# Kernel tuning notes

Measured on AMD Instinct MI355X. Metric: run time of the kernel, lower is better.

Reference implementation:

```python
import jax, jax.numpy as jnp
import numpy as np

N_NODES = 100000
N_EDGES = 1600000
D_IN = 128
D_HID = 128
D_OUT = 128


def setup_inputs() -> dict:
    key = jax.random.key(0)
    ks = jax.random.split(key, 12)
    x = jax.random.normal(ks[0], (N_NODES, D_IN), dtype=jnp.float32)
    edge_index = jax.random.randint(ks[1], (2, N_EDGES), 0, N_NODES, dtype=jnp.int64)
    s = 0.05
    # GraphConv layer l: out = agg @ w_rel + x @ w_root + b  (lin_rel has bias, lin_root does not)
    w_rel1 = jax.random.normal(ks[2], (D_IN, D_HID), dtype=jnp.float32) * s
    w_root1 = jax.random.normal(ks[3], (D_IN, D_HID), dtype=jnp.float32) * s
    b1 = jax.random.normal(ks[4], (D_HID,), dtype=jnp.float32) * s
    w_rel2 = jax.random.normal(ks[5], (D_HID, D_HID), dtype=jnp.float32) * s
    w_root2 = jax.random.normal(ks[6], (D_HID, D_HID), dtype=jnp.float32) * s
    b2 = jax.random.normal(ks[7], (D_HID,), dtype=jnp.float32) * s
    w_rel3 = jax.random.normal(ks[8], (D_HID, D_OUT), dtype=jnp.float32) * s
    w_root3 = jax.random.normal(ks[9], (D_HID, D_OUT), dtype=jnp.float32) * s
    b3 = jax.random.normal(ks[10], (D_OUT,), dtype=jnp.float32) * s
    return {"x": x, "edge_index": edge_index,
            "w_rel1": w_rel1, "w_root1": w_root1, "b1": b1,
            "w_rel2": w_rel2, "w_root2": w_root2, "b2": b2,
            "w_rel3": w_rel3, "w_root3": w_root3, "b3": b3}


def _graph_conv(h, src, dst, w_rel, w_root, b):
    # sum-aggregate neighbor features (message = x_j, flow src -> dst),
    # then linear; identical math to PyG GraphConv with aggr='add'.
    agg = jax.ops.segment_sum(h[src], dst, num_segments=h.shape[0])
    return agg @ w_rel + h @ w_root + b


def reference(x, edge_index, w_rel1, w_root1, b1, w_rel2, w_root2, b2, w_rel3, w_root3, b3):
    src, dst = edge_index[0], edge_index[1]
    h = jax.nn.relu(_graph_conv(x, src, dst, w_rel1, w_root1, b1))
    h = jax.nn.relu(_graph_conv(h, src, dst, w_rel2, w_root2, b2))
    out = _graph_conv(h, src, dst, w_rel3, w_root3, b3)
    return out
```

## Files before the change

kernel.cpp:

```cpp
#include <hip/hip_runtime.h>
#include <hip/hip_bf16.h>
#include <stdint.h>

typedef __hip_bfloat16 bf16;
typedef __hip_bfloat162 bf162;

typedef __attribute__((ext_vector_type(8))) short short8;
typedef __attribute__((ext_vector_type(4))) float floatx4;

#define BSH   8
#define BSZ   256
#define CHUNK 8192
#define NBMAX 512


__device__ __forceinline__ void acc2(float& a, float& b, unsigned u) {
    a += __uint_as_float(u << 16);
    b += __uint_as_float(u & 0xffff0000u);
}

__global__ __launch_bounds__(256)
void prep_bhist_kernel(const float* __restrict__ x, bf16* __restrict__ y, int n4, int nCvt,
                       const float* __restrict__ wr1, const float* __restrict__ wo1,
                       const float* __restrict__ wr2, const float* __restrict__ wo2,
                       const float* __restrict__ wr3, const float* __restrict__ wo3,
                       bf16* __restrict__ w1, bf16* __restrict__ w2, bf16* __restrict__ w3,
                       const int* __restrict__ dst, int* __restrict__ T,
                       int E, int NB, int GB) {
    __shared__ int lh[NBMAX];
    const int b = blockIdx.x;
    if (b < nCvt) {
        const int i = b * 256 + threadIdx.x;
        if (i < n4) {
            float4 v = ((const float4*)x)[i];
            bf162 a, c;
            a.x = __float2bfloat16(v.x); a.y = __float2bfloat16(v.y);
            c.x = __float2bfloat16(v.z); c.y = __float2bfloat16(v.w);
            ((bf162*)y)[i * 2]     = a;
            ((bf162*)y)[i * 2 + 1] = c;
        }
        return;
    }
    if (b < nCvt + 48) {
        int t = (b - nCvt) * 256 + threadIdx.x;
        const int layer = t >> 12;
        t &= 4095;
        const float* wrel  = (layer == 0) ? wr1 : (layer == 1) ? wr2 : wr3;
        const float* wroot = (layer == 0) ? wo1 : (layer == 1) ? wo2 : wo3;
        bf16*        wsw   = (layer == 0) ? w1  : (layer == 1) ? w2  : w3;
        const int lane = t & 63;
        const int ct   = (t >> 6) & 7;
        const int kt   = t >> 9;
        const int kbase = kt * 32 + (lane >> 4) * 8;
        const int n     = ct * 16 + (lane & 15);
        bf16* q = wsw + (size_t)t * 8;
#pragma unroll
        for (int j = 0; j < 8; ++j) {
            const int k = kbase + j;
            const float v = (k < 128) ? wrel[k * 128 + n] : wroot[(k - 128) * 128 + n];
            q[j] = __float2bfloat16(v);
        }
        return;
    }
    const int bb = b - nCvt - 48;
    for (int u = threadIdx.x; u < NB; u += 256) lh[u] = 0;
    __syncthreads();
    const int beg = bb * CHUNK, end = min(beg + CHUNK, E);
    for (int e = beg + threadIdx.x; e < end; e += 256)
        atomicAdd(&lh[dst[e] >> BSH], 1);
    __syncthreads();
    for (int u = threadIdx.x; u < NB; u += 256)
        T[u * GB + bb] = lh[u];
}


__global__ __launch_bounds__(256)
void scan1_kernel(const int* __restrict__ deg, int* __restrict__ rp,
                  int* __restrict__ bsum, int n) {
    __shared__ int s[256];
    const int tid = threadIdx.x;
    const int i = blockIdx.x * 256 + tid;
    const int d = (i < n) ? deg[i] : 0;
    s[tid] = d;
    __syncthreads();
    for (int off = 1; off < 256; off <<= 1) {
        int u = (tid >= off) ? s[tid - off] : 0;
        __syncthreads();
        s[tid] += u;
        __syncthreads();
    }
    if (i < n) rp[i] = s[tid] - d;
    if (tid == 255) bsum[blockIdx.x] = s[255];
}

__global__ __launch_bounds__(512)
void scan2_kernel(int* __restrict__ bsum, int G) {
    __shared__ int s[512];
    const int tid = threadIdx.x;
    const int d = (tid < G) ? bsum[tid] : 0;
    s[tid] = d;
    __syncthreads();
    for (int off = 1; off < 512; off <<= 1) {
        int u = (tid >= off) ? s[tid - off] : 0;
        __syncthreads();
        s[tid] += u;
        __syncthreads();
    }
    if (tid < G) bsum[tid] = s[tid] - d;
}


__global__ __launch_bounds__(256)
void bscatter_kernel(const int* __restrict__ src, const int* __restrict__ dst,
                     const int* __restrict__ T, const int* __restrict__ bsum,
                     int* __restrict__ ebuf, int E, int NB, int GB) {
    __shared__ int lofs[NBMAX];
    const int b = blockIdx.x;
    for (int u = threadIdx.x; u < NB; u += 256) {
        const int idx = u * GB + b;
        lofs[u] = T[idx] + bsum[idx >> 8];
    }
    __syncthreads();
    const int beg = b * CHUNK, end = min(beg + CHUNK, E);
    for (int e = beg + threadIdx.x; e < end; e += 256) {
        const int d = dst[e];
        const int u = d >> BSH;
        const int pos = atomicAdd(&lofs[u], 1);
        ebuf[pos] = (src[e] << BSH) | (d & (BSZ - 1));
    }
}

__global__ __launch_bounds__(256)
void bbuild_kernel(const int* __restrict__ T, const int* __restrict__ bsum,
                   const int* __restrict__ ebuf,
                   int* __restrict__ rp, int* __restrict__ col,
                   int E, int N, int NB, int GB) {
    __shared__ int s[256];
    __shared__ int lrank[256];
    const int u = blockIdx.x;
    const int tid = threadIdx.x;
    const int i0 = u * GB;
    const int beg = T[i0] + bsum[i0 >> 8];
    const int i1 = (u + 1) * GB;
    const int end = (u + 1 < NB) ? (T[i1] + bsum[i1 >> 8]) : E;

    lrank[tid] = 0;
    __syncthreads();
    for (int e = beg + tid; e < end; e += 256)
        atomicAdd(&lrank[ebuf[e] & (BSZ - 1)], 1);
    __syncthreads();
    const int cntv = lrank[tid];
    s[tid] = cntv;
    __syncthreads();
    for (int off = 1; off < 256; off <<= 1) {
        int v = (tid >= off) ? s[tid - off] : 0;
        __syncthreads();
        s[tid] += v;
        __syncthreads();
    }
    const int excl = s[tid] - cntv;
    const int node = u * BSZ + tid;
    if (node < N) rp[node] = beg + excl;
    if (u == NB - 1 && tid == 0) rp[N] = E;
    lrank[tid] = beg + excl;
    __syncthreads();
    for (int e = beg + tid; e < end; e += 256) {
        const int p = ebuf[e];
        const int pos = atomicAdd(&lrank[p & (BSZ - 1)], 1);
        col[pos] = p >> BSH;
    }
}


__global__ __launch_bounds__(512)
void agg_kernel(const bf16* __restrict__ h, const int* __restrict__ rp,
                const int* __restrict__ col, bf16* __restrict__ agg, int N) {
    const int lane = threadIdx.x & 63;
    const int wid  = threadIdx.x >> 6;
    const int node = blockIdx.x * 8 + wid;
    if (node >= N) return;
    const int half = lane >> 5;
    const int l32  = lane & 31;
    const int f    = l32 * 4;
    const int beg = rp[node], end = rp[node + 1];

    float acc[4] = {0.f, 0.f, 0.f, 0.f};
    int e = beg;
#pragma unroll 2
    for (; e + 8 <= end; e += 8) {
        const int s0 = col[e + half];
        const int s1 = col[e + 2 + half];
        const int s2 = col[e + 4 + half];
        const int s3 = col[e + 6 + half];
        const uint2 r0 = *(const uint2*)(h + (size_t)s0 * 128 + f);
        const uint2 r1 = *(const uint2*)(h + (size_t)s1 * 128 + f);
        const uint2 r2 = *(const uint2*)(h + (size_t)s2 * 128 + f);
        const uint2 r3 = *(const uint2*)(h + (size_t)s3 * 128 + f);
        acc2(acc[0], acc[1], r0.x); acc2(acc[2], acc[3], r0.y);
        acc2(acc[0], acc[1], r1.x); acc2(acc[2], acc[3], r1.y);
        acc2(acc[0], acc[1], r2.x); acc2(acc[2], acc[3], r2.y);
        acc2(acc[0], acc[1], r3.x); acc2(acc[2], acc[3], r3.y);
    }
    for (; e < end; e += 2) {
        const bool act = (e + half) < end;
        const int s = col[act ? (e + half) : e];
        const uint2 r = *(const uint2*)(h + (size_t)s * 128 + f);
        if (act) { acc2(acc[0], acc[1], r.x); acc2(acc[2], acc[3], r.y); }
    }
#pragma unroll
    for (int j = 0; j < 4; ++j)
        acc[j] += __shfl_xor(acc[j], 32, 64);
    if (half == 0) {
        bf162 o0, o1;
        o0.x = __float2bfloat16(acc[0]); o0.y = __float2bfloat16(acc[1]);
        o1.x = __float2bfloat16(acc[2]); o1.y = __float2bfloat16(acc[3]);
        bf162* q = (bf162*)(agg + (size_t)node * 128 + f);
        q[0] = o0;
        q[1] = o1;
    }
}


template <bool RELU, typename OT>
__global__ __launch_bounds__(512)
void mfma_gemm_kernel(const bf16* __restrict__ Aagg, const bf16* __restrict__ Hroot,
                      const bf16* __restrict__ wsw, const float* __restrict__ bias,
                      OT* __restrict__ out, int M) {
    __shared__ __align__(16) char smem[67584];
    const int tid = threadIdx.x;

#pragma unroll
    for (int i = 0; i < 8; ++i) {
        const int off = i * 8192 + tid * 16;
        *(float4*)(smem + off) = *(const float4*)((const char*)wsw + off);
    }
    __syncthreads();

    const int lane = tid & 63;
    const int wave = tid >> 6;
    const int l15  = lane & 15;
    const int quad = lane >> 4;
    const int base = blockIdx.x * 128;
    const int row_a = base + wave * 16 + l15;
    const bool rowok = row_a < M;
    const bf16* wl = (const bf16*)smem;

    floatx4 acc[8];
#pragma unroll
    for (int ct = 0; ct < 8; ++ct) acc[ct] = (floatx4){0.f, 0.f, 0.f, 0.f};

#pragma unroll
    for (int kt = 0; kt < 8; ++kt) {
        const bf16* Abase = (kt < 4) ? Aagg : Hroot;
        const int k0 = (kt & 3) * 32 + quad * 8;
        short8 afrag = (short8){0, 0, 0, 0, 0, 0, 0, 0};
        if (rowok) afrag = *(const short8*)(Abase + (size_t)row_a * 128 + k0);
#pragma unroll
        for (int ct = 0; ct < 8; ++ct) {
            const short8 bfrag = *(const short8*)(wl + (size_t)((kt * 8 + ct) * 64 + lane) * 8);
            acc[ct] = __builtin_amdgcn_mfma_f32_16x16x32_bf16(afrag, bfrag, acc[ct], 0, 0, 0);
        }
    }

    __syncthreads();
    const int rloc = wave * 16 + quad * 4;

    if constexpr (sizeof(OT) == 2) {
        bf16* tl = (bf16*)smem;
#pragma unroll
        for (int ct = 0; ct < 8; ++ct) {
            const int colc = ct * 16 + l15;
            const float bv = bias[colc];
#pragma unroll
            for (int r = 0; r < 4; ++r) {
                float v = acc[ct][r] + bv;
                if (RELU) v = fmaxf(v, 0.f);
                tl[(rloc + r) * 136 + colc] = __float2bfloat16(v);
            }
        }
        __syncthreads();
#pragma unroll
        for (int i = 0; i < 4; ++i) {
            const int chunk = i * 512 + tid;
            const int row = chunk >> 4;
            const int c   = chunk & 15;
            if (base + row < M)
                *(float4*)((char*)out + (size_t)(base + row) * 256 + c * 16) =
                    *(const float4*)(smem + row * 272 + c * 16);
        }
    } else {
        float* tl = (float*)smem;
#pragma unroll
        for (int ct = 0; ct < 8; ++ct) {
            const int colc = ct * 16 + l15;
            const float bv = bias[colc];
#pragma unroll
            for (int r = 0; r < 4; ++r) {
                float v = acc[ct][r] + bv;
                if (RELU) v = fmaxf(v, 0.f);
                tl[(rloc + r) * 132 + colc] = v;
            }
        }
        __syncthreads();
#pragma unroll
        for (int i = 0; i < 8; ++i) {
            const int chunk = i * 512 + tid;
            const int row = chunk >> 5;
            const int c   = chunk & 31;
            if (base + row < M)
                *(float4*)((char*)out + (size_t)(base + row) * 512 + c * 16) =
                    *(const float4*)(smem + row * 528 + c * 16);
        }
    }
}


extern "C" void kernel_launch(void* const* d_in, const int* in_sizes, int n_in,
                              void* d_out, int out_size, void* d_ws, size_t ws_size,
                              hipStream_t stream) {
    const float* x       = (const float*)d_in[0];
    const int*   ei      = (const int*)d_in[1];
    const float* w_rel1  = (const float*)d_in[2];
    const float* w_root1 = (const float*)d_in[3];
    const float* b1      = (const float*)d_in[4];
    const float* w_rel2  = (const float*)d_in[5];
    const float* w_root2 = (const float*)d_in[6];
    const float* b2      = (const float*)d_in[7];
    const float* w_rel3  = (const float*)d_in[8];
    const float* w_root3 = (const float*)d_in[9];
    const float* b3      = (const float*)d_in[10];
    float* out = (float*)d_out;

    const int N = in_sizes[0] / 128;
    const int E = in_sizes[1] / 2;
    const int* src = ei;
    const int* dst = ei + E;

    char* w = (char*)d_ws;
    auto alloc = [&](size_t bytes) {
        char* p = w;
        w += (bytes + 255) & ~(size_t)255;
        return p;
    };
    int*  col  = (int*)alloc((size_t)E * 4);
    int*  rp   = (int*)alloc((size_t)(N + 1) * 4);
    bf16* h1   = (bf16*)alloc((size_t)N * 128 * 2);
    bf16* xbf  = (bf16*)alloc((size_t)N * 128 * 2);
    bf16* aggb = (bf16*)alloc((size_t)N * 128 * 2);
    bf16* wsw1 = (bf16*)alloc(32768 * 2);
    bf16* wsw2 = (bf16*)alloc(32768 * 2);
    bf16* wsw3 = (bf16*)alloc(32768 * 2);
    bf16* h2   = xbf;
    int*  T    = (int*)h1;
    int*  bsum = (int*)(h1 + 1024 * 1024);
    int*  ebuf = (int*)aggb;

    const int NB = (N + BSZ - 1) / BSZ;
    const int GB = (E + CHUNK - 1) / CHUNK;
    const int nT = NB * GB;
    const int scanTBlocks = (nT + 255) / 256;

    const int aggBlocks  = (N + 7) / 8;
    const int gemmBlocks = (N + 127) / 128;
    const int cvtBlocks  = (N * 32 + 255) / 256;

    prep_bhist_kernel<<<cvtBlocks + 48 + GB, 256, 0, stream>>>(
        x, xbf, N * 32, cvtBlocks,
        w_rel1, w_root1, w_rel2, w_root2, w_rel3, w_root3,
        wsw1, wsw2, wsw3,
        dst, T, E, NB, GB);

    scan1_kernel<<<scanTBlocks, 256, 0, stream>>>(T, T, bsum, nT);
    scan2_kernel<<<1, 512, 0, stream>>>(bsum, scanTBlocks);
    bscatter_kernel<<<GB, 256, 0, stream>>>(src, dst, T, bsum, ebuf, E, NB, GB);
    bbuild_kernel<<<NB, 256, 0, stream>>>(T, bsum, ebuf, rp, col, E, N, NB, GB);

    agg_kernel<<<aggBlocks, 512, 0, stream>>>(xbf, rp, col, aggb, N);
    mfma_gemm_kernel<true, bf16><<<gemmBlocks, 512, 0, stream>>>(aggb, xbf, wsw1, b1, h1, N);
    agg_kernel<<<aggBlocks, 512, 0, stream>>>(h1, rp, col, aggb, N);
    mfma_gemm_kernel<true, bf16><<<gemmBlocks, 512, 0, stream>>>(aggb, h1, wsw2, b2, h2, N);
    agg_kernel<<<aggBlocks, 512, 0, stream>>>(h2, rp, col, aggb, N);
    mfma_gemm_kernel<false, float><<<gemmBlocks, 512, 0, stream>>>(aggb, h2, wsw3, b3, out, N);
}
```

Baseline: 425.9 us.

## Store bf16 features in 16-column slabs so each aggregation block gathers from one slab

```diff
diff --git a/kernel.cpp b/kernel.cpp
--- a/kernel.cpp
+++ b/kernel.cpp
@@ -12,6 +12,8 @@
 #define BSZ   256
 #define CHUNK 8192
 #define NBMAX 512
+#define NSLAB 8
+
 
 
 __device__ __forceinline__ void acc2(float& a, float& b, unsigned u) {
@@ -32,12 +34,16 @@
     if (b < nCvt) {
         const int i = b * 256 + threadIdx.x;
         if (i < n4) {
+            const int N = n4 >> 5;
+            const int n = i >> 5;
+            const int q = i & 31;
             float4 v = ((const float4*)x)[i];
-            bf162 a, c;
-            a.x = __float2bfloat16(v.x); a.y = __float2bfloat16(v.y);
-            c.x = __float2bfloat16(v.z); c.y = __float2bfloat16(v.w);
-            ((bf162*)y)[i * 2]     = a;
-            ((bf162*)y)[i * 2 + 1] = c;
+            union { bf16 bb[4]; unsigned long long u; } pk;
+            pk.bb[0] = __float2bfloat16(v.x);
+            pk.bb[1] = __float2bfloat16(v.y);
+            pk.bb[2] = __float2bfloat16(v.z);
+            pk.bb[3] = __float2bfloat16(v.w);
+            *(unsigned long long*)(y + ((size_t)(q >> 2) * N + n) * 16 + (q & 3) * 4) = pk.u;
         }
         return;
     }
@@ -175,49 +181,42 @@
 __global__ __launch_bounds__(512)
 void agg_kernel(const bf16* __restrict__ h, const int* __restrict__ rp,
                 const int* __restrict__ col, bf16* __restrict__ agg, int N) {
-    const int lane = threadIdx.x & 63;
-    const int wid  = threadIdx.x >> 6;
-    const int node = blockIdx.x * 8 + wid;
+    const int s    = blockIdx.x & 7;
+    const int tid  = threadIdx.x;
+    const int wid  = tid >> 6;
+    const int lane = tid & 63;
+    const int g    = lane >> 2;
+    const int fl   = lane & 3;
+    const int node = (blockIdx.x >> 3) * 128 + wid * 16 + g;
     if (node >= N) return;
-    const int half = lane >> 5;
-    const int l32  = lane & 31;
-    const int f    = l32 * 4;
+
+    const bf16* Hs = h + (size_t)s * N * 16;
     const int beg = rp[node], end = rp[node + 1];
 
-    float acc[4] = {0.f, 0.f, 0.f, 0.f};
+    float a0 = 0.f, a1 = 0.f, a2 = 0.f, a3 = 0.f;
     int e = beg;
 #pragma unroll 2
-    for (; e + 8 <= end; e += 8) {
-        const int s0 = col[e + half];
-        const int s1 = col[e + 2 + half];
-        const int s2 = col[e + 4 + half];
-        const int s3 = col[e + 6 + half];
-        const uint2 r0 = *(const uint2*)(h + (size_t)s0 * 128 + f);
-        const uint2 r1 = *(const uint2*)(h + (size_t)s1 * 128 + f);
-        const uint2 r2 = *(const uint2*)(h + (size_t)s2 * 128 + f);
-        const uint2 r3 = *(const uint2*)(h + (size_t)s3 * 128 + f);
-        acc2(acc[0], acc[1], r0.x); acc2(acc[2], acc[3], r0.y);
-        acc2(acc[0], acc[1], r1.x); acc2(acc[2], acc[3], r1.y);
-        acc2(acc[0], acc[1], r2.x); acc2(acc[2], acc[3], r2.y);
-        acc2(acc[0], acc[1], r3.x); acc2(acc[2], acc[3], r3.y);
-    }
-    for (; e < end; e += 2) {
-        const bool act = (e + half) < end;
-        const int s = col[act ? (e + half) : e];
-        const uint2 r = *(const uint2*)(h + (size_t)s * 128 + f);
-        if (act) { acc2(acc[0], acc[1], r.x); acc2(acc[2], acc[3], r.y); }
-    }
-#pragma unroll
-    for (int j = 0; j < 4; ++j)
-        acc[j] += __shfl_xor(acc[j], 32, 64);
-    if (half == 0) {
-        bf162 o0, o1;
-        o0.x = __float2bfloat16(acc[0]); o0.y = __float2bfloat16(acc[1]);
-        o1.x = __float2bfloat16(acc[2]); o1.y = __float2bfloat16(acc[3]);
-        bf162* q = (bf162*)(agg + (size_t)node * 128 + f);
-        q[0] = o0;
-        q[1] = o1;
-    }
+    for (; e + 2 <= end; e += 2) {
+        const int s0 = col[e];
+        const int s1 = col[e + 1];
+        const uint2 r0 = *(const uint2*)(Hs + (size_t)s0 * 16 + fl * 4);
+        const uint2 r1 = *(const uint2*)(Hs + (size_t)s1 * 16 + fl * 4);
+        acc2(a0, a1, r0.x); acc2(a2, a3, r0.y);
+        acc2(a0, a1, r1.x); acc2(a2, a3, r1.y);
+    }
+    if (e < end) {
+        const int s0 = col[e];
+        const uint2 r0 = *(const uint2*)(Hs + (size_t)s0 * 16 + fl * 4);
+        acc2(a0, a1, r0.x); acc2(a2, a3, r0.y);
+    }
+
+    union { bf16 bb[4]; unsigned long long u; } pk;
+    pk.bb[0] = __float2bfloat16(a0);
+    pk.bb[1] = __float2bfloat16(a1);
+    pk.bb[2] = __float2bfloat16(a2);
+    pk.bb[3] = __float2bfloat16(a3);
+    __builtin_nontemporal_store(pk.u,
+        (unsigned long long*)(agg + ((size_t)s * N + node) * 16 + fl * 4));
 }
 
 
@@ -254,7 +253,8 @@
         const bf16* Abase = (kt < 4) ? Aagg : Hroot;
         const int k0 = (kt & 3) * 32 + quad * 8;
         short8 afrag = (short8){0, 0, 0, 0, 0, 0, 0, 0};
-        if (rowok) afrag = *(const short8*)(Abase + (size_t)row_a * 128 + k0);
+        if (rowok)
+            afrag = *(const short8*)(Abase + ((size_t)(k0 >> 4) * M + row_a) * 16 + (k0 & 15));
 #pragma unroll
         for (int ct = 0; ct < 8; ++ct) {
             const short8 bfrag = *(const short8*)(wl + (size_t)((kt * 8 + ct) * 64 + lane) * 8);
@@ -282,11 +282,12 @@
 #pragma unroll
         for (int i = 0; i < 4; ++i) {
             const int chunk = i * 512 + tid;
-            const int row = chunk >> 4;
-            const int c   = chunk & 15;
-            if (base + row < M)
-                *(float4*)((char*)out + (size_t)(base + row) * 256 + c * 16) =
-                    *(const float4*)(smem + row * 272 + c * 16);
+            const int slab = chunk >> 8;
+            const int r    = (chunk >> 1) & 127;
+            const int half = chunk & 1;
+            if (base + r < M)
+                *(float4*)((char*)out + ((size_t)slab * M + base + r) * 32 + half * 16) =
+                    *(const float4*)(smem + r * 272 + slab * 32 + half * 16);
         }
     } else {
         float* tl = (float*)smem;
@@ -360,7 +361,7 @@
     const int nT = NB * GB;
     const int scanTBlocks = (nT + 255) / 256;
 
-    const int aggBlocks  = (N + 7) / 8;
+    const int aggBlocks  = 8 * ((N + 127) / 128);
     const int gemmBlocks = (N + 127) / 128;
     const int cvtBlocks  = (N * 32 + 255) / 256;
 
```

Result: slower. 479.3 us (+12.5%).

## Fuse CSR-build preprocessing stages into one cooperative persistent kernel

Applied to the files above, without the earlier changes.

```diff
diff --git a/kernel.cpp b/kernel.cpp
--- a/kernel.cpp
+++ b/kernel.cpp
@@ -1,4 +1,5 @@
 #include <hip/hip_runtime.h>
+#include <hip/hip_cooperative_groups.h>
 #include <hip/hip_bf16.h>
 #include <stdint.h>
 
@@ -18,6 +19,168 @@
     a += __uint_as_float(u << 16);
     b += __uint_as_float(u & 0xffff0000u);
 }
+
+__device__ __forceinline__ void wsw_prep_one(int t,
+        const float* wr1, const float* wo1, const float* wr2, const float* wo2,
+        const float* wr3, const float* wo3, bf16* w1, bf16* w2, bf16* w3) {
+    const int layer = t >> 12;
+    t &= 4095;
+    const float* wrel  = (layer == 0) ? wr1 : (layer == 1) ? wr2 : wr3;
+    const float* wroot = (layer == 0) ? wo1 : (layer == 1) ? wo2 : wo3;
+    bf16*        wsw   = (layer == 0) ? w1  : (layer == 1) ? w2  : w3;
+    const int lane = t & 63;
+    const int ct   = (t >> 6) & 7;
+    const int kt   = t >> 9;
+    const int kbase = kt * 32 + (lane >> 4) * 8;
+    const int n     = ct * 16 + (lane & 15);
+    bf16* q = wsw + (size_t)t * 8;
+#pragma unroll
+    for (int j = 0; j < 8; ++j) {
+        const int k = kbase + j;
+        const float v = (k < 128) ? wrel[k * 128 + n] : wroot[(k - 128) * 128 + n];
+        q[j] = __float2bfloat16(v);
+    }
+}
+
+
+struct FrontArgs {
+    const float* x;
+    const int*   ei;
+    const float *wr1, *wo1, *wr2, *wo2, *wr3, *wo3;
+    bf16 *xbf, *wsw1, *wsw2, *wsw3;
+    int  *T, *bsum, *rp, *col, *ebuf;
+    int N, E, NB, GB, nT;
+};
+
+__global__ __launch_bounds__(256)
+void front_kernel(FrontArgs a) {
+    namespace cg = cooperative_groups;
+    cg::grid_group grid = cg::this_grid();
+    __shared__ int lh[NBMAX];
+    __shared__ int ls[256];
+
+    const int tid  = threadIdx.x;
+    const int G    = gridDim.x;
+    const int gtid = blockIdx.x * 256 + tid;
+    const int gsz  = G * 256;
+    const int* src = a.ei;
+    const int* dst = a.ei + a.E;
+
+    const int n4 = a.N * 32;
+    for (int i = gtid; i < n4; i += gsz) {
+        float4 v = ((const float4*)a.x)[i];
+        bf162 p, q;
+        p.x = __float2bfloat16(v.x); p.y = __float2bfloat16(v.y);
+        q.x = __float2bfloat16(v.z); q.y = __float2bfloat16(v.w);
+        ((bf162*)a.xbf)[i * 2]     = p;
+        ((bf162*)a.xbf)[i * 2 + 1] = q;
+    }
+    for (int t = gtid; t < 3 * 4096; t += gsz)
+        wsw_prep_one(t, a.wr1, a.wo1, a.wr2, a.wo2, a.wr3, a.wo3,
+                     a.wsw1, a.wsw2, a.wsw3);
+    for (int c = blockIdx.x; c < a.GB; c += G) {
+        for (int u = tid; u < a.NB; u += 256) lh[u] = 0;
+        __syncthreads();
+        const int beg = c * CHUNK, end = min(beg + CHUNK, a.E);
+        for (int e = beg + tid; e < end; e += 256)
+            atomicAdd(&lh[dst[e] >> BSH], 1);
+        __syncthreads();
+        for (int u = tid; u < a.NB; u += 256) a.T[u * a.GB + c] = lh[u];
+        __syncthreads();
+    }
+    grid.sync();
+
+    const int nChunk = (a.nT + 255) >> 8;
+    for (int c = blockIdx.x; c < nChunk; c += G) {
+        const int i = c * 256 + tid;
+        const int d = (i < a.nT) ? a.T[i] : 0;
+        ls[tid] = d;
+        __syncthreads();
+        for (int off = 1; off < 256; off <<= 1) {
+            int u = (tid >= off) ? ls[tid - off] : 0;
+            __syncthreads();
+            ls[tid] += u;
+            __syncthreads();
+        }
+        if (i < a.nT) a.T[i] = ls[tid] - d;
+        if (tid == 255) a.bsum[c] = ls[255];
+        __syncthreads();
+    }
+    grid.sync();
+
+    if (blockIdx.x == 0) {
+        int carry = 0;
+        for (int off = 0; off < nChunk; off += 256) {
+            const int i = off + tid;
+            const int v = (i < nChunk) ? a.bsum[i] : 0;
+            ls[tid] = v;
+            __syncthreads();
+            for (int d2 = 1; d2 < 256; d2 <<= 1) {
+                int u = (tid >= d2) ? ls[tid - d2] : 0;
+                __syncthreads();
+                ls[tid] += u;
+                __syncthreads();
+            }
+            if (i < nChunk) a.bsum[i] = carry + ls[tid] - v;
+            const int tot = ls[255];
+            __syncthreads();
+            carry += tot;
+        }
+    }
+    grid.sync();
+
+    for (int c = blockIdx.x; c < a.GB; c += G) {
+        for (int u = tid; u < a.NB; u += 256) {
+            const int idx = u * a.GB + c;
+            lh[u] = a.T[idx] + a.bsum[idx >> 8];
+        }
+        __syncthreads();
+        const int beg = c * CHUNK, end = min(beg + CHUNK, a.E);
+        for (int e = beg + tid; e < end; e += 256) {
+            const int d = dst[e];
+            const int u = d >> BSH;
+            const int pos = atomicAdd(&lh[u], 1);
+            a.ebuf[pos] = (src[e] << BSH) | (d & (BSZ - 1));
+        }
+        __syncthreads();
+    }
+    grid.sync();
+
+    for (int u = blockIdx.x; u < a.NB; u += G) {
+        const int i0 = u * a.GB;
+        const int beg = a.T[i0] + a.bsum[i0 >> 8];
+        const int i1 = (u + 1) * a.GB;
+        const int end = (u + 1 < a.NB) ? (a.T[i1] + a.bsum[i1 >> 8]) : a.E;
+        lh[tid] = 0;
+        __syncthreads();
+        for (int e = beg + tid; e < end; e += 256)
+            atomicAdd(&lh[a.ebuf[e] & (BSZ - 1)], 1);
+        __syncthreads();
+        const int cntv = lh[tid];
+        ls[tid] = cntv;
+        __syncthreads();
+        for (int off = 1; off < 256; off <<= 1) {
+            int v = (tid >= off) ? ls[tid - off] : 0;
+            __syncthreads();
+            ls[tid] += v;
+            __syncthreads();
+        }
+        const int excl = ls[tid] - cntv;
+        const int node = u * BSZ + tid;
+        if (node < a.N) a.rp[node] = beg + excl;
+        if (u == a.NB - 1 && tid == 0) a.rp[a.N] = a.E;
+        __syncthreads();
+        lh[tid] = beg + excl;
+        __syncthreads();
+        for (int e = beg + tid; e < end; e += 256) {
+            const int p = a.ebuf[e];
+            const int pos = atomicAdd(&lh[p & (BSZ - 1)], 1);
+            a.col[pos] = p >> BSH;
+        }
+        __syncthreads();
+    }
+}
+
 
 __global__ __launch_bounds__(256)
 void prep_bhist_kernel(const float* __restrict__ x, bf16* __restrict__ y, int n4, int nCvt,
@@ -42,24 +205,8 @@
         return;
     }
     if (b < nCvt + 48) {
-        int t = (b - nCvt) * 256 + threadIdx.x;
-        const int layer = t >> 12;
-        t &= 4095;
-        const float* wrel  = (layer == 0) ? wr1 : (layer == 1) ? wr2 : wr3;
-        const float* wroot = (layer == 0) ? wo1 : (layer == 1) ? wo2 : wo3;
-        bf16*        wsw   = (layer == 0) ? w1  : (layer == 1) ? w2  : w3;
-        const int lane = t & 63;
-        const int ct   = (t >> 6) & 7;
-        const int kt   = t >> 9;
-        const int kbase = kt * 32 + (lane >> 4) * 8;
-        const int n     = ct * 16 + (lane & 15);
-        bf16* q = wsw + (size_t)t * 8;
-#pragma unroll
-        for (int j = 0; j < 8; ++j) {
-            const int k = kbase + j;
-            const float v = (k < 128) ? wrel[k * 128 + n] : wroot[(k - 128) * 128 + n];
-            q[j] = __float2bfloat16(v);
-        }
+        wsw_prep_one((b - nCvt) * 256 + threadIdx.x,
+                     wr1, wo1, wr2, wo2, wr3, wo3, w1, w2, w3);
         return;
     }
     const int bb = b - nCvt - 48;
@@ -72,7 +219,6 @@
     for (int u = threadIdx.x; u < NB; u += 256)
         T[u * GB + bb] = lh[u];
 }
-
 
 __global__ __launch_bounds__(256)
 void scan1_kernel(const int* __restrict__ deg, int* __restrict__ rp,
@@ -108,7 +254,6 @@
     }
     if (tid < G) bsum[tid] = s[tid] - d;
 }
-
 
 __global__ __launch_bounds__(256)
 void bscatter_kernel(const int* __restrict__ src, const int* __restrict__ dst,
@@ -222,7 +367,7 @@
 
 
 template <bool RELU, typename OT>
-__global__ __launch_bounds__(512)
+__global__ __launch_bounds__(512, 4)
 void mfma_gemm_kernel(const bf16* __restrict__ Aagg, const bf16* __restrict__ Hroot,
                       const bf16* __restrict__ wsw, const float* __restrict__ bias,
                       OT* __restrict__ out, int M) {
@@ -364,16 +509,45 @@
     const int gemmBlocks = (N + 127) / 128;
     const int cvtBlocks  = (N * 32 + 255) / 256;
 
-    prep_bhist_kernel<<<cvtBlocks + 48 + GB, 256, 0, stream>>>(
-        x, xbf, N * 32, cvtBlocks,
-        w_rel1, w_root1, w_rel2, w_root2, w_rel3, w_root3,
-        wsw1, wsw2, wsw3,
-        dst, T, E, NB, GB);
-
-    scan1_kernel<<<scanTBlocks, 256, 0, stream>>>(T, T, bsum, nT);
-    scan2_kernel<<<1, 512, 0, stream>>>(bsum, scanTBlocks);
-    bscatter_kernel<<<GB, 256, 0, stream>>>(src, dst, T, bsum, ebuf, E, NB, GB);
-    bbuild_kernel<<<NB, 256, 0, stream>>>(T, bsum, ebuf, rp, col, E, N, NB, GB);
+    static int frontGrid = 0;
+    if (frontGrid == 0) {
+        int perCU = 0, nCU = 0, dev = 0;
+        hipError_t e1 = hipGetDevice(&dev);
+        hipError_t e2 = hipDeviceGetAttribute(&nCU, hipDeviceAttributeMultiprocessorCount, dev);
+        hipError_t e3 = hipOccupancyMaxActiveBlocksPerMultiprocessor(&perCU, front_kernel, 256, 0);
+        if (e1 == hipSuccess && e2 == hipSuccess && e3 == hipSuccess && perCU > 0 && nCU > 0) {
+            frontGrid = perCU * nCU;
+            if (frontGrid > 512) frontGrid = 512;
+        } else {
+            frontGrid = -1;
+        }
+    }
+
+    bool frontDone = false;
+    if (frontGrid > 0) {
+        FrontArgs fa;
+        fa.x = x; fa.ei = ei;
+        fa.wr1 = w_rel1; fa.wo1 = w_root1; fa.wr2 = w_rel2; fa.wo2 = w_root2;
+        fa.wr3 = w_rel3; fa.wo3 = w_root3;
+        fa.xbf = xbf; fa.wsw1 = wsw1; fa.wsw2 = wsw2; fa.wsw3 = wsw3;
+        fa.T = T; fa.bsum = bsum; fa.rp = rp; fa.col = col; fa.ebuf = ebuf;
+        fa.N = N; fa.E = E; fa.NB = NB; fa.GB = GB; fa.nT = nT;
+        void* args[] = {&fa};
+        if (hipLaunchCooperativeKernel((const void*)front_kernel, dim3(frontGrid),
+                                       dim3(256), args, 0, stream) == hipSuccess)
+            frontDone = true;
+    }
+    if (!frontDone) {
+        prep_bhist_kernel<<<cvtBlocks + 48 + GB, 256, 0, stream>>>(
+            x, xbf, N * 32, cvtBlocks,
+            w_rel1, w_root1, w_rel2, w_root2, w_rel3, w_root3,
+            wsw1, wsw2, wsw3,
+            dst, T, E, NB, GB);
+        scan1_kernel<<<scanTBlocks, 256, 0, stream>>>(T, T, bsum, nT);
+        scan2_kernel<<<1, 512, 0, stream>>>(bsum, scanTBlocks);
+        bscatter_kernel<<<GB, 256, 0, stream>>>(src, dst, T, bsum, ebuf, E, NB, GB);
+        bbuild_kernel<<<NB, 256, 0, stream>>>(T, bsum, ebuf, rp, col, E, N, NB, GB);
+    }
 
     agg_kernel<<<aggBlocks, 512, 0, stream>>>(xbf, rp, col, aggb, N);
     mfma_gemm_kernel<true, bf16><<<gemmBlocks, 512, 0, stream>>>(aggb, xbf, wsw1, b1, h1, N);
```

Measured after the change: 678.2 us. 59.2% more time.
